# Kernel optimization log

Hardware: AMD Instinct MI355X
Metric: run time of the kernel (lower is better)

Reference implementation:

```python
import jax, jax.numpy as jnp
import numpy as np

K = 64            # number of keypoints
PATCH = 16        # patch size
NUM_CLASSES = 1000
K_HARRIS = 0.04


def _conv3x3(x, w):
    # x: [N, Cin, H, W], w: [Cout, Cin, 3, 3], stride 1, padding 1 (torch conv2d = cross-correlation)
    return jax.lax.conv_general_dilated(x, w, (1, 1), 'SAME',
                                        dimension_numbers=('NCHW', 'OIHW', 'NCHW'))


def _harris_coords(x, k, patch_size):
    B, C, H, W = x.shape
    g = jnp.mean(x, axis=1, keepdims=True) if C != 1 else x  # grayscale [B,1,H,W]
    dxk = jnp.array([[-1., 0., 1.], [-1., 0., 1.], [-1., 0., 1.]], x.dtype).reshape(1, 1, 3, 3)
    dyk = jnp.array([[-1., -1., -1.], [0., 0., 0.], [1., 1., 1.]], x.dtype).reshape(1, 1, 3, 3)
    gauss = (jnp.array([[1., 2., 1.], [2., 4., 2.], [1., 2., 1.]], x.dtype) / 16.0).reshape(1, 1, 3, 3)
    dx = _conv3x3(g, dxk)
    dy = _conv3x3(g, dyk)
    Sxx = _conv3x3(dx * dx, gauss)
    Syy = _conv3x3(dy * dy, gauss)
    Sxy = _conv3x3(dx * dy, gauss)
    R = Sxx * Syy - Sxy ** 2 - K_HARRIS * (Sxx + Syy) ** 2  # [B,1,H,W]
    m = patch_size
    mask = jnp.zeros((H, W), x.dtype).at[m:H - m, m:W - m].set(1.0)
    R_flat = (R[:, 0] * mask).reshape(B, -1)
    _, idx = jax.lax.top_k(R_flat, k)                        # [B,k]
    coords = jnp.stack([idx // W, idx % W], axis=-1).astype(jnp.float32)  # (row, col)
    coords = (coords / jnp.array([H, W], jnp.float32) - 0.5) * 2.0
    return jnp.clip(coords, -1.0, 1.0)                       # [B,k,2]


def _grid_sample_bilinear(img, grid):
    # img: [N,C,H,W]; grid: [N,Hg,Wg,2] with (x, y) in [-1,1]; align_corners=True, zeros padding
    N, C, H, W = img.shape
    Hg, Wg = grid.shape[1], grid.shape[2]
    gx = (grid[..., 0] + 1.0) * 0.5 * (W - 1)
    gy = (grid[..., 1] + 1.0) * 0.5 * (H - 1)
    x0 = jnp.floor(gx); y0 = jnp.floor(gy)
    x1 = x0 + 1.0;      y1 = y0 + 1.0
    wx1 = gx - x0; wx0 = 1.0 - wx1
    wy1 = gy - y0; wy0 = 1.0 - wy1

    img_flat = img.reshape(N, C, H * W)

    def gather(xi, yi):
        valid = ((xi >= 0) & (xi < W) & (yi >= 0) & (yi < H)).astype(img.dtype)
        xc = jnp.clip(xi, 0, W - 1).astype(jnp.int32)
        yc = jnp.clip(yi, 0, H - 1).astype(jnp.int32)
        flat = (yc * W + xc).reshape(N, 1, Hg * Wg)
        vals = jnp.take_along_axis(img_flat, flat, axis=2).reshape(N, C, Hg, Wg)
        return vals * valid[:, None]

    out = (gather(x0, y0) * (wx0 * wy0)[:, None]
           + gather(x1, y0) * (wx1 * wy0)[:, None]
           + gather(x0, y1) * (wx0 * wy1)[:, None]
           + gather(x1, y1) * (wx1 * wy1)[:, None])
    return out


def _extract_patches(images, keypoints, patch_size):
    B, C, H, W = images.shape
    k = keypoints.shape[1]
    coords01 = (keypoints + 1.0) / 2.0                       # [B,k,2] (y,x) in [0,1]
    r = patch_size / H
    pg = jnp.linspace(-r, r, patch_size)
    yy, xx = jnp.meshgrid(pg, pg, indexing='ij')
    base = jnp.stack([xx, yy], axis=-1)[None, None]          # [1,1,P,P,2] (x_off, y_off)
    grid = base + coords01[:, :, None, None, :]              # faithful to original broadcast
    grid = grid * 2.0 - 1.0
    grid = grid.reshape(B * k, patch_size, patch_size, 2)
    x_exp = jnp.repeat(images, k, axis=0)                    # repeat_interleave on batch
    patches = _grid_sample_bilinear(x_exp, grid)             # [B*k,C,P,P]
    return patches.reshape(B, k, C, patch_size, patch_size)


def _classify(patches, conv_w, conv_b, fc1_w, fc1_b, fc2_w, fc2_b):
    B, k, C, H, W = patches.shape
    p = patches.reshape(B * k, C, H, W)
    h = _conv3x3(p, conv_w) + conv_b[None, :, None, None]
    h = jax.nn.relu(h)
    h = h.reshape(B * k, -1)                                 # [B*k, 8*P*P]
    h = jax.nn.relu(h @ fc1_w.T + fc1_b)                     # [B*k, 64]
    h = h.reshape(B, k * 64)
    return h @ fc2_w.T + fc2_b                               # [B, num_classes]


def setup_inputs() -> dict:
    key = jax.random.key(0)
    ks = jax.random.split(key, 7)
    B, C, H, W = 32, 3, 224, 224
    return {
        'x': jax.random.normal(ks[0], (B, C, H, W), dtype=jnp.float32),
        'conv_w': jax.random.normal(ks[1], (8, C, 3, 3), dtype=jnp.float32) * 0.1,
        'conv_b': jax.random.normal(ks[2], (8,), dtype=jnp.float32) * 0.05,
        'fc1_w': jax.random.normal(ks[3], (64, 8 * PATCH * PATCH), dtype=jnp.float32) * 0.02,
        'fc1_b': jax.random.normal(ks[4], (64,), dtype=jnp.float32) * 0.05,
        'fc2_w': jax.random.normal(ks[5], (NUM_CLASSES, 64 * K), dtype=jnp.float32) * 0.02,
        'fc2_b': jax.random.normal(ks[6], (NUM_CLASSES,), dtype=jnp.float32) * 0.05,
    }


def reference(x, conv_w, conv_b, fc1_w, fc1_b, fc2_w, fc2_b):
    coords = _harris_coords(x, K, PATCH)                     # [B,K,2]
    patches = _extract_patches(x, coords, PATCH)             # [B,K,C,P,P]
    return _classify(patches, conv_w, conv_b, fc1_w, fc1_b, fc2_w, fc2_b)
```

## Files before the change

kernel.cpp:

```cpp
#include <hip/hip_runtime.h>
#include <cstdint>
#include <math.h>

#define HW 224
#define NPIX (HW*HW)
#define BATCH 32
#define KP 64
#define PS 16
#define NCLS 1000
#define TKW 112
#define FC1_KS 16

__device__ __forceinline__ uint64_t tk_pack(float v, int idx) {
    uint32_t u = __float_as_uint(v);
    u = (u & 0x80000000u) ? ~u : (u | 0x80000000u);
    return ((uint64_t)u << 32) | (uint32_t)(~idx);
}

__device__ __forceinline__ uint64_t tk_sort_asc(uint64_t k, int lane) {
    #pragma unroll
    for (int size = 2; size <= 64; size <<= 1) {
        #pragma unroll
        for (int stride = size >> 1; stride >= 1; stride >>= 1) {
            uint64_t o = __shfl_xor(k, stride, 64);
            bool up = ((lane & size) == 0);
            bool keepmax = (((lane & stride) != 0) == up);
            k = keepmax ? (k > o ? k : o) : (k < o ? k : o);
        }
    }
    return k;
}

__device__ __forceinline__ uint64_t tk_clean_desc(uint64_t k, int lane) {
    #pragma unroll
    for (int stride = 32; stride >= 1; stride >>= 1) {
        uint64_t o = __shfl_xor(k, stride, 64);
        bool keepmax = ((lane & stride) == 0);
        k = keepmax ? (k > o ? k : o) : (k < o ? k : o);
    }
    return k;
}

__global__ __launch_bounds__(256) void k_harris_topk(const float* __restrict__ x,
                                                     uint64_t* __restrict__ cand) {
    const int r = blockIdx.x, b = blockIdx.y;
    const int tid = threadIdx.x;
    const int row0 = r * 8;
    __shared__ float G[12][228];
    __shared__ float DXs[10][228];
    __shared__ float DYs[10][228];
    __shared__ float RB[1792];
    const float* xb = x + (size_t)b * 3 * NPIX;

    for (int l = tid; l < 12 * 224; l += 256) {
        int gr = l / 224, gc = l % 224;
        int gy = row0 - 2 + gr;
        float v = 0.f;
        if (gy >= 0 && gy < HW) {
            int o = gy * HW + gc;
            v = (xb[o] + xb[NPIX + o] + xb[2 * NPIX + o]) / 3.0f;
        }
        G[gr][gc + 1] = v;
    }
    if (tid < 12) { G[tid][0] = 0.f; G[tid][225] = 0.f; }
    if (tid < 10) { DXs[tid][0] = 0.f; DXs[tid][225] = 0.f;
                    DYs[tid][0] = 0.f; DYs[tid][225] = 0.f; }
    __syncthreads();

    for (int l = tid; l < 10 * 224; l += 256) {
        int dr = l / 224, dc = l % 224;
        int ay = row0 - 1 + dr;
        float dxv = 0.f, dyv = 0.f;
        if (ay >= 0 && ay < HW) {
            dxv = (G[dr][dc + 2] - G[dr][dc]) + (G[dr + 1][dc + 2] - G[dr + 1][dc]) +
                  (G[dr + 2][dc + 2] - G[dr + 2][dc]);
            dyv = (G[dr + 2][dc] + G[dr + 2][dc + 1] + G[dr + 2][dc + 2]) -
                  (G[dr][dc] + G[dr][dc + 1] + G[dr][dc + 2]);
        }
        DXs[dr][dc + 1] = dxv;
        DYs[dr][dc + 1] = dyv;
    }
    __syncthreads();

    for (int l = tid; l < 1792; l += 256) {
        int rr = l / 224, c = l % 224;
        int gy = row0 + rr;
        float outv = 0.f;
        if (gy >= PS && gy < HW - PS && c >= PS && c < HW - PS) {
            const float gw[3][3] = {{1.f/16.f, 2.f/16.f, 1.f/16.f},
                                    {2.f/16.f, 4.f/16.f, 2.f/16.f},
                                    {1.f/16.f, 2.f/16.f, 1.f/16.f}};
            float sxx = 0.f, syy = 0.f, sxy = 0.f;
            #pragma unroll
            for (int u = 0; u < 3; u++)
                #pragma unroll
                for (int v = 0; v < 3; v++) {
                    float dv = DXs[rr + u][c + v];
                    float ev = DYs[rr + u][c + v];
                    float w = gw[u][v];
                    sxx += w * dv * dv;
                    syy += w * ev * ev;
                    sxy += w * dv * ev;
                }
            float tr = sxx + syy;
            outv = sxx * syy - sxy * sxy - 0.04f * tr * tr;
        }
        RB[l] = outv;
    }
    __syncthreads();

    const int w = tid >> 6, lane = tid & 63;
    const int chunk = w * 448;
    const int gbase = row0 * 224 + chunk;
    uint64_t T = 0;
    #pragma unroll 1
    for (int it = 0; it < 7; it++) {
        float v = RB[chunk + it * 64 + lane];
        uint64_t ck = tk_pack(v, gbase + it * 64 + lane);
        uint64_t thr = __shfl(T, 63, 64);
        if (__ballot(ck > thr)) {
            uint64_t s = tk_sort_asc(ck, lane);
            uint64_t m = (T > s) ? T : s;
            T = tk_clean_desc(m, lane);
        }
    }
    cand[((size_t)b * TKW + r * 4 + w) * 64 + lane] = T;
}

__global__ __launch_bounds__(1024) void k_topk_merge(const uint64_t* __restrict__ cand,
                                                     int* __restrict__ kp) {
    const int img = blockIdx.x;
    const int w = threadIdx.x >> 6, lane = threadIdx.x & 63;
    const uint64_t* cb = cand + (size_t)img * TKW * 64;
    __shared__ uint64_t S[16 * 64];

    uint64_t T = cb[(w * 7) * 64 + lane];
    #pragma unroll
    for (int r = 1; r < 7; r++) {
        uint64_t C = cb[(w * 7 + r) * 64 + (63 - lane)];
        uint64_t m = (T > C) ? T : C;
        T = tk_clean_desc(m, lane);
    }
    S[w * 64 + lane] = T;
    __syncthreads();
    if (w == 0) {
        uint64_t T2 = S[lane];
        #pragma unroll
        for (int r = 1; r < 16; r++) {
            uint64_t C = S[r * 64 + (63 - lane)];
            uint64_t m = (T2 > C) ? T2 : C;
            T2 = tk_clean_desc(m, lane);
        }
        kp[img * KP + lane] = (int)(~(uint32_t)T2);
    }
}

__device__ __forceinline__ float gat4(const float* img, float xf, float yf) {
    bool valid = (xf >= 0.f) && (xf < 224.f) && (yf >= 0.f) && (yf < 224.f);
    if (!valid) return 0.f;
    int xi = (int)fminf(fmaxf(xf, 0.f), 223.f);
    int yi = (int)fminf(fmaxf(yf, 0.f), 223.f);
    return img[yi * HW + xi];
}

__global__ __launch_bounds__(256) void k_patch_conv(
    const float* __restrict__ x, const int* __restrict__ kp,
    const float* __restrict__ conv_w, const float* __restrict__ conv_b,
    float* __restrict__ h) {
    const int s = blockIdx.x;
    const int b = blockIdx.y;
    const int tid = threadIdx.x;

    __shared__ float P[3][16][16];
    __shared__ float CW[216];
    __shared__ float CB[8];
    for (int l = tid; l < 216; l += 256) CW[l] = conv_w[l];
    if (tid < 8) CB[tid] = conv_b[tid];

    const int idx = kp[b * KP + s];
    const int row = idx / HW, col = idx % HW;
    float cy = ((float)row / 224.0f - 0.5f) * 2.0f;
    float cx = ((float)col / 224.0f - 0.5f) * 2.0f;
    cy = fminf(fmaxf(cy, -1.0f), 1.0f);
    cx = fminf(fmaxf(cx, -1.0f), 1.0f);
    const float y01 = (cy + 1.0f) * 0.5f;
    const float x01 = (cx + 1.0f) * 0.5f;
    const float rr = 16.0f / 224.0f;
    const float step = (2.0f * rr) / 15.0f;
    const float* xb = x + (size_t)b * 3 * NPIX;

    for (int e = tid; e < 768; e += 256) {
        int c = e >> 8, rem = e & 255, i = rem >> 4, j = rem & 15;
        float pj = (j == 15) ? rr : (-rr + (float)j * step);
        float pi = (i == 15) ? rr : (-rr + (float)i * step);
        float gxn = (pj + y01) * 2.0f - 1.0f;
        float gyn = (pi + x01) * 2.0f - 1.0f;
        float gx = (gxn + 1.0f) * 0.5f * 223.0f;
        float gy = (gyn + 1.0f) * 0.5f * 223.0f;
        float x0 = floorf(gx), y0 = floorf(gy);
        float x1 = x0 + 1.0f, y1 = y0 + 1.0f;
        float wx1 = gx - x0, wy1 = gy - y0;
        float wx0 = 1.0f - wx1, wy0 = 1.0f - wy1;
        const float* img = xb + (size_t)c * NPIX;
        float acc = gat4(img, x0, y0) * (wx0 * wy0)
                  + gat4(img, x1, y0) * (wx1 * wy0)
                  + gat4(img, x0, y1) * (wx0 * wy1)
                  + gat4(img, x1, y1) * (wx1 * wy1);
        P[c][i][j] = acc;
    }
    __syncthreads();

    const int i = tid >> 4, j = tid & 15;
    const size_t mbase = ((size_t)(b * KP + s)) * 2048;
    #pragma unroll
    for (int co = 0; co < 8; co++) {
        float acc = CB[co];
        #pragma unroll
        for (int ci = 0; ci < 3; ci++)
            #pragma unroll
            for (int di = 0; di < 3; di++)
                #pragma unroll
                for (int dj = 0; dj < 3; dj++) {
                    int yy = i + di - 1, xx = j + dj - 1;
                    if (yy >= 0 && yy < 16 && xx >= 0 && xx < 16)
                        acc += P[ci][yy][xx] * CW[co * 27 + ci * 9 + di * 3 + dj];
                }
        h[mbase + co * 256 + tid] = fmaxf(acc, 0.0f);
    }
}

__global__ __launch_bounds__(256) void k_fc1(
    const float* __restrict__ h, const float* __restrict__ fc1_w,
    float* __restrict__ partial) {
    const int mt = blockIdx.x;
    const int ks = blockIdx.y;
    const int tid = threadIdx.x;
    const int M0 = mt * 64;
    const int og = tid >> 4, mg = tid & 15;
    __shared__ float A[64 * 68];
    __shared__ float W[64 * 68];
    float acc[4][4];
    #pragma unroll
    for (int i = 0; i < 4; i++)
        #pragma unroll
        for (int j = 0; j < 4; j++) acc[i][j] = 0.f;

    #pragma unroll 1
    for (int ch = 0; ch < 2; ch++) {
        const int k0 = ks * 128 + ch * 64;
        __syncthreads();
        #pragma unroll
        for (int p = 0; p < 4; p++) {
            int row = p * 16 + (tid >> 4);
            int c0 = (tid & 15) * 4;
            float4 av = *(const float4*)&h[(size_t)(M0 + row) * 2048 + k0 + c0];
            A[(c0 + 0) * 68 + row] = av.x;
            A[(c0 + 1) * 68 + row] = av.y;
            A[(c0 + 2) * 68 + row] = av.z;
            A[(c0 + 3) * 68 + row] = av.w;
            float4 wv = *(const float4*)&fc1_w[(size_t)row * 2048 + k0 + c0];
            W[(c0 + 0) * 68 + row] = wv.x;
            W[(c0 + 1) * 68 + row] = wv.y;
            W[(c0 + 2) * 68 + row] = wv.z;
            W[(c0 + 3) * 68 + row] = wv.w;
        }
        __syncthreads();
        #pragma unroll 4
        for (int k = 0; k < 64; k++) {
            float4 a = *(float4*)&A[k * 68 + mg * 4];
            float4 w = *(float4*)&W[k * 68 + og * 4];
            acc[0][0] += a.x * w.x; acc[0][1] += a.x * w.y;
            acc[0][2] += a.x * w.z; acc[0][3] += a.x * w.w;
            acc[1][0] += a.y * w.x; acc[1][1] += a.y * w.y;
            acc[1][2] += a.y * w.z; acc[1][3] += a.y * w.w;
            acc[2][0] += a.z * w.x; acc[2][1] += a.z * w.y;
            acc[2][2] += a.z * w.z; acc[2][3] += a.z * w.w;
            acc[3][0] += a.w * w.x; acc[3][1] += a.w * w.y;
            acc[3][2] += a.w * w.z; acc[3][3] += a.w * w.w;
        }
    }
    float* pb = partial + ((size_t)ks * 2048 + M0) * 64;
    #pragma unroll
    for (int mi = 0; mi < 4; mi++) {
        float4 v = make_float4(acc[mi][0], acc[mi][1], acc[mi][2], acc[mi][3]);
        *(float4*)&pb[(mg * 4 + mi) * 64 + og * 4] = v;
    }
}

__global__ __launch_bounds__(256) void k_fc1_post(
    const float* __restrict__ partial, const float* __restrict__ fc1_b,
    const float* __restrict__ fc2_b, float* __restrict__ featT,
    float* __restrict__ out) {
    const int id = blockIdx.x * 256 + threadIdx.x;
    const int o = id & 63, m = id >> 6;
    float s = 0.f;
    #pragma unroll
    for (int ks = 0; ks < FC1_KS; ks++) s += partial[(size_t)ks * 131072 + id];
    s = fmaxf(s + fc1_b[o], 0.f);
    featT[(size_t)((m & 63) * 64 + o) * 32 + (m >> 6)] = s;
    if (id < BATCH * NCLS) out[id] = fc2_b[id % NCLS];
}

__global__ __launch_bounds__(256) void k_fc2(
    const float* __restrict__ featT, const float* __restrict__ fc2_w,
    float* __restrict__ out) {
    const int c0 = blockIdx.x * 8;
    const int kbase = blockIdx.y * 256;
    const int tid = threadIdx.x;
    const int b = tid & 31, kg = tid >> 5;
    __shared__ float F[128 * 36];
    __shared__ float Wc[8 * 128];
    __shared__ float Red[8 * 8 * 32];

    float acc[8];
    #pragma unroll
    for (int cl = 0; cl < 8; cl++) acc[cl] = 0.f;

    #pragma unroll 1
    for (int ch = 0; ch < 2; ch++) {
        const int k0 = kbase + ch * 128;
        __syncthreads();
        #pragma unroll
        for (int r = 0; r < 4; r++) {
            int l = tid + r * 256;
            int f = l >> 3, b4 = (l & 7) << 2;
            *(float4*)&F[f * 36 + b4] =
                *(const float4*)&featT[(size_t)(k0 + f) * 32 + b4];
        }
        {
            int cl = tid >> 5, koff = (tid & 31) << 2;
            *(float4*)&Wc[cl * 128 + koff] =
                *(const float4*)&fc2_w[(size_t)(c0 + cl) * 4096 + k0 + koff];
        }
        __syncthreads();
        #pragma unroll
        for (int cl = 0; cl < 8; cl++) {
            #pragma unroll
            for (int i = 0; i < 16; i += 4) {
                float4 wv = *(float4*)&Wc[cl * 128 + kg * 16 + i];
                int f = kg * 16 + i;
                acc[cl] += wv.x * F[f * 36 + b] + wv.y * F[(f + 1) * 36 + b] +
                           wv.z * F[(f + 2) * 36 + b] + wv.w * F[(f + 3) * 36 + b];
            }
        }
    }
    __syncthreads();
    #pragma unroll
    for (int cl = 0; cl < 8; cl++) Red[(kg * 8 + cl) * 32 + b] = acc[cl];
    __syncthreads();
    const int cl2 = tid >> 5, b2 = tid & 31;
    float s = 0.f;
    #pragma unroll
    for (int g = 0; g < 8; g++) s += Red[(g * 8 + cl2) * 32 + b2];
    atomicAdd(&out[b2 * NCLS + c0 + cl2], s);
}

extern "C" void kernel_launch(void* const* d_in, const int* in_sizes, int n_in,
                              void* d_out, int out_size, void* d_ws, size_t ws_size,
                              hipStream_t stream) {
    const float* x      = (const float*)d_in[0];
    const float* conv_w = (const float*)d_in[1];
    const float* conv_b = (const float*)d_in[2];
    const float* fc1_w  = (const float*)d_in[3];
    const float* fc1_b  = (const float*)d_in[4];
    const float* fc2_w  = (const float*)d_in[5];
    const float* fc2_b  = (const float*)d_in[6];
    float* out = (float*)d_out;

    char* base = (char*)d_ws;
    const size_t region0 = (size_t)FC1_KS * 2048 * 64 * 4;
    uint64_t* cand    = (uint64_t*)base;
    float*    partial = (float*)base;
    float*    h       = (float*)(base + region0);
    float*    featT   = h + (size_t)2048 * 2048;
    int*      kp      = (int*)(featT + (size_t)4096 * 32);

    k_harris_topk<<<dim3(28, 32), 256, 0, stream>>>(x, cand);
    k_topk_merge<<<32, 1024, 0, stream>>>(cand, kp);
    k_patch_conv<<<dim3(KP, BATCH), 256, 0, stream>>>(x, kp, conv_w, conv_b, h);
    k_fc1<<<dim3(32, FC1_KS), 256, 0, stream>>>(h, fc1_w, partial);
    k_fc1_post<<<512, 256, 0, stream>>>(partial, fc1_b, fc2_b, featT, out);
    k_fc2<<<dim3(125, 16), 256, 0, stream>>>(featT, fc2_w, out);
}
```

Baseline: 187.9 us.

## Zero-pad patch tile, register-block conv, and retile fc2 over natural feature layout

The patch conv kernel now stores an 18x18 zero-padded patch in shared memory. This removes the bounds checks in the 3x3 conv, and each thread loads its 9 neighbours once per input channel and reuses them across all 8 output channels, reading weights straight from global/constant memory. fc1_post writes features in their natural [B, K*64] layout instead of a transposed scatter. fc2 is retiled so each thread computes a 4-batch by 8-class block with float4 LDS reads, followed by a wider 32-way shared-memory reduction. The risks are more reduction work and possible LDS bank conflicts in the new tiling.

```diff
diff --git a/kernel.cpp b/kernel.cpp
--- a/kernel.cpp
+++ b/kernel.cpp
@@ -171,11 +171,7 @@
     const int b = blockIdx.y;
     const int tid = threadIdx.x;
 
-    __shared__ float P[3][16][16];
-    __shared__ float CW[216];
-    __shared__ float CB[8];
-    for (int l = tid; l < 216; l += 256) CW[l] = conv_w[l];
-    if (tid < 8) CB[tid] = conv_b[tid];
+    __shared__ float P[3][18][18];
 
     const int idx = kp[b * KP + s];
     const int row = idx / HW, col = idx % HW;
@@ -189,44 +185,57 @@
     const float step = (2.0f * rr) / 15.0f;
     const float* xb = x + (size_t)b * 3 * NPIX;
 
-    for (int e = tid; e < 768; e += 256) {
-        int c = e >> 8, rem = e & 255, i = rem >> 4, j = rem & 15;
-        float pj = (j == 15) ? rr : (-rr + (float)j * step);
-        float pi = (i == 15) ? rr : (-rr + (float)i * step);
-        float gxn = (pj + y01) * 2.0f - 1.0f;
-        float gyn = (pi + x01) * 2.0f - 1.0f;
-        float gx = (gxn + 1.0f) * 0.5f * 223.0f;
-        float gy = (gyn + 1.0f) * 0.5f * 223.0f;
-        float x0 = floorf(gx), y0 = floorf(gy);
-        float x1 = x0 + 1.0f, y1 = y0 + 1.0f;
-        float wx1 = gx - x0, wy1 = gy - y0;
-        float wx0 = 1.0f - wx1, wy0 = 1.0f - wy1;
-        const float* img = xb + (size_t)c * NPIX;
-        float acc = gat4(img, x0, y0) * (wx0 * wy0)
-                  + gat4(img, x1, y0) * (wx1 * wy0)
-                  + gat4(img, x0, y1) * (wx0 * wy1)
-                  + gat4(img, x1, y1) * (wx1 * wy1);
-        P[c][i][j] = acc;
+    for (int e = tid; e < 972; e += 256) {
+        int c = e / 324, rem = e - c * 324;
+        int yy = rem / 18, xx = rem - yy * 18;
+        float val = 0.f;
+        if (yy >= 1 && yy <= 16 && xx >= 1 && xx <= 16) {
+            int i = yy - 1, j = xx - 1;
+            float pj = (j == 15) ? rr : (-rr + (float)j * step);
+            float pi = (i == 15) ? rr : (-rr + (float)i * step);
+            float gxn = (pj + y01) * 2.0f - 1.0f;
+            float gyn = (pi + x01) * 2.0f - 1.0f;
+            float gx = (gxn + 1.0f) * 0.5f * 223.0f;
+            float gy = (gyn + 1.0f) * 0.5f * 223.0f;
+            float x0 = floorf(gx), y0 = floorf(gy);
+            float x1 = x0 + 1.0f, y1 = y0 + 1.0f;
+            float wx1 = gx - x0, wy1 = gy - y0;
+            float wx0 = 1.0f - wx1, wy0 = 1.0f - wy1;
+            const float* img = xb + (size_t)c * NPIX;
+            val = gat4(img, x0, y0) * (wx0 * wy0)
+                + gat4(img, x1, y0) * (wx1 * wy0)
+                + gat4(img, x0, y1) * (wx0 * wy1)
+                + gat4(img, x1, y1) * (wx1 * wy1);
+        }
+        P[c][yy][xx] = val;
     }
     __syncthreads();
 
     const int i = tid >> 4, j = tid & 15;
+    float acc[8];
+    #pragma unroll
+    for (int co = 0; co < 8; co++) acc[co] = conv_b[co];
+    #pragma unroll
+    for (int ci = 0; ci < 3; ci++) {
+        float n[9];
+        #pragma unroll
+        for (int di = 0; di < 3; di++)
+            #pragma unroll
+            for (int dj = 0; dj < 3; dj++)
+                n[di * 3 + dj] = P[ci][i + di][j + dj];
+        #pragma unroll
+        for (int co = 0; co < 8; co++) {
+            float a = acc[co];
+            #pragma unroll
+            for (int u = 0; u < 9; u++)
+                a += n[u] * conv_w[co * 27 + ci * 9 + u];
+            acc[co] = a;
+        }
+    }
     const size_t mbase = ((size_t)(b * KP + s)) * 2048;
     #pragma unroll
-    for (int co = 0; co < 8; co++) {
-        float acc = CB[co];
-        #pragma unroll
-        for (int ci = 0; ci < 3; ci++)
-            #pragma unroll
-            for (int di = 0; di < 3; di++)
-                #pragma unroll
-                for (int dj = 0; dj < 3; dj++) {
-                    int yy = i + di - 1, xx = j + dj - 1;
-                    if (yy >= 0 && yy < 16 && xx >= 0 && xx < 16)
-                        acc += P[ci][yy][xx] * CW[co * 27 + ci * 9 + di * 3 + dj];
-                }
-        h[mbase + co * 256 + tid] = fmaxf(acc, 0.0f);
-    }
+    for (int co = 0; co < 8; co++)
+        h[mbase + co * 256 + tid] = fmaxf(acc[co], 0.0f);
 }
 
 __global__ __launch_bounds__(256) void k_fc1(
@@ -289,69 +298,76 @@
 
 __global__ __launch_bounds__(256) void k_fc1_post(
     const float* __restrict__ partial, const float* __restrict__ fc1_b,
-    const float* __restrict__ fc2_b, float* __restrict__ featT,
+    const float* __restrict__ fc2_b, float* __restrict__ feat,
     float* __restrict__ out) {
     const int id = blockIdx.x * 256 + threadIdx.x;
-    const int o = id & 63, m = id >> 6;
+    const int o = id & 63;
     float s = 0.f;
     #pragma unroll
     for (int ks = 0; ks < FC1_KS; ks++) s += partial[(size_t)ks * 131072 + id];
     s = fmaxf(s + fc1_b[o], 0.f);
-    featT[(size_t)((m & 63) * 64 + o) * 32 + (m >> 6)] = s;
+    feat[id] = s;
     if (id < BATCH * NCLS) out[id] = fc2_b[id % NCLS];
 }
 
 __global__ __launch_bounds__(256) void k_fc2(
-    const float* __restrict__ featT, const float* __restrict__ fc2_w,
+    const float* __restrict__ feat, const float* __restrict__ fc2_w,
     float* __restrict__ out) {
     const int c0 = blockIdx.x * 8;
     const int kbase = blockIdx.y * 256;
     const int tid = threadIdx.x;
-    const int b = tid & 31, kg = tid >> 5;
-    __shared__ float F[128 * 36];
-    __shared__ float Wc[8 * 128];
-    __shared__ float Red[8 * 8 * 32];
-
-    float acc[8];
-    #pragma unroll
-    for (int cl = 0; cl < 8; cl++) acc[cl] = 0.f;
+    const int bq = tid & 7, kg = tid >> 3;
+
+    __shared__ float U[8192];
+    float* F2 = U;
+    float* Wc = U + 32 * 132;
+    float* Red = U;
+
+    float4 acc[8];
+    #pragma unroll
+    for (int cl = 0; cl < 8; cl++) acc[cl] = make_float4(0.f, 0.f, 0.f, 0.f);
 
     #pragma unroll 1
     for (int ch = 0; ch < 2; ch++) {
         const int k0 = kbase + ch * 128;
         __syncthreads();
         #pragma unroll
-        for (int r = 0; r < 4; r++) {
-            int l = tid + r * 256;
-            int f = l >> 3, b4 = (l & 7) << 2;
-            *(float4*)&F[f * 36 + b4] =
-                *(const float4*)&featT[(size_t)(k0 + f) * 32 + b4];
+        for (int it = 0; it < 4; it++) {
+            int l = it * 256 + tid;
+            int bb = l >> 5, kc = (l & 31) << 2;
+            *(float4*)&F2[bb * 132 + kc] =
+                *(const float4*)&feat[(size_t)bb * 4096 + k0 + kc];
         }
         {
-            int cl = tid >> 5, koff = (tid & 31) << 2;
-            *(float4*)&Wc[cl * 128 + koff] =
-                *(const float4*)&fc2_w[(size_t)(c0 + cl) * 4096 + k0 + koff];
+            int cl = tid >> 5, kc = (tid & 31) << 2;
+            *(float4*)&Wc[cl * 128 + kc] =
+                *(const float4*)&fc2_w[(size_t)(c0 + cl) * 4096 + k0 + kc];
         }
         __syncthreads();
+        float4 f0 = *(float4*)&F2[(bq * 4 + 0) * 132 + kg * 4];
+        float4 f1 = *(float4*)&F2[(bq * 4 + 1) * 132 + kg * 4];
+        float4 f2 = *(float4*)&F2[(bq * 4 + 2) * 132 + kg * 4];
+        float4 f3 = *(float4*)&F2[(bq * 4 + 3) * 132 + kg * 4];
         #pragma unroll
         for (int cl = 0; cl < 8; cl++) {
-            #pragma unroll
-            for (int i = 0; i < 16; i += 4) {
-                float4 wv = *(float4*)&Wc[cl * 128 + kg * 16 + i];
-                int f = kg * 16 + i;
-                acc[cl] += wv.x * F[f * 36 + b] + wv.y * F[(f + 1) * 36 + b] +
-                           wv.z * F[(f + 2) * 36 + b] + wv.w * F[(f + 3) * 36 + b];
-            }
-        }
-    }
-    __syncthreads();
-    #pragma unroll
-    for (int cl = 0; cl < 8; cl++) Red[(kg * 8 + cl) * 32 + b] = acc[cl];
-    __syncthreads();
+            float4 w = *(float4*)&Wc[cl * 128 + kg * 4];
+            acc[cl].x += w.x * f0.x + w.y * f0.y + w.z * f0.z + w.w * f0.w;
+            acc[cl].y += w.x * f1.x + w.y * f1.y + w.z * f1.z + w.w * f1.w;
+            acc[cl].z += w.x * f2.x + w.y * f2.y + w.z * f2.z + w.w * f2.w;
+            acc[cl].w += w.x * f3.x + w.y * f3.y + w.z * f3.z + w.w * f3.w;
+        }
+    }
+
+    __syncthreads();
+    #pragma unroll
+    for (int cl = 0; cl < 8; cl++)
+        *(float4*)&Red[kg * 256 + cl * 32 + bq * 4] = acc[cl];
+    __syncthreads();
+
     const int cl2 = tid >> 5, b2 = tid & 31;
     float s = 0.f;
     #pragma unroll
-    for (int g = 0; g < 8; g++) s += Red[(g * 8 + cl2) * 32 + b2];
+    for (int g = 0; g < 32; g++) s += Red[g * 256 + cl2 * 32 + b2];
     atomicAdd(&out[b2 * NCLS + c0 + cl2], s);
 }
 
@@ -372,13 +388,13 @@
     uint64_t* cand    = (uint64_t*)base;
     float*    partial = (float*)base;
     float*    h       = (float*)(base + region0);
-    float*    featT   = h + (size_t)2048 * 2048;
-    int*      kp      = (int*)(featT + (size_t)4096 * 32);
+    float*    feat    = h + (size_t)2048 * 2048;
+    int*      kp      = (int*)(feat + (size_t)4096 * 32);
 
     k_harris_topk<<<dim3(28, 32), 256, 0, stream>>>(x, cand);
     k_topk_merge<<<32, 1024, 0, stream>>>(cand, kp);
     k_patch_conv<<<dim3(KP, BATCH), 256, 0, stream>>>(x, kp, conv_w, conv_b, h);
     k_fc1<<<dim3(32, FC1_KS), 256, 0, stream>>>(h, fc1_w, partial);
-    k_fc1_post<<<512, 256, 0, stream>>>(partial, fc1_b, fc2_b, featT, out);
-    k_fc2<<<dim3(125, 16), 256, 0, stream>>>(featT, fc2_w, out);
-}
+    k_fc1_post<<<512, 256, 0, stream>>>(partial, fc1_b, fc2_b, feat, out);
+    k_fc2<<<dim3(125, 16), 256, 0, stream>>>(feat, fc2_w, out);
+}
```

Result: faster. 171.2 us (-8.9%).
